# Optimization experiments

Measured on AMD Instinct MI355X. Metric: run time of the kernel, lower is better.

## Reference

```python
import jax, jax.numpy as jnp
import numpy as np

B, S, D, H = 2, 2048, 1024, 16
DK = D // H


def setup_inputs() -> dict:
    key = jax.random.key(0)
    ks = jax.random.split(key, 12)
    s = 0.02
    return {
        "q": jax.random.normal(ks[0], (B, S, D), jnp.float32),
        "k": jax.random.normal(ks[1], (B, S, D), jnp.float32),
        "v": jax.random.normal(ks[2], (B, S, D), jnp.float32),
        "mask": jax.random.randint(ks[3], (1, 1, S, S), 0, 2, jnp.int32),
        "Wq": jax.random.normal(ks[4], (D, D), jnp.float32) * s,
        "bq": jnp.zeros((D,), jnp.float32),
        "Wk": jax.random.normal(ks[5], (D, D), jnp.float32) * s,
        "bk": jnp.zeros((D,), jnp.float32),
        "Wv": jax.random.normal(ks[6], (D, D), jnp.float32) * s,
        "bv": jnp.zeros((D,), jnp.float32),
        "Wo": jax.random.normal(ks[7], (D, D), jnp.float32) * s,
        "bo": jnp.zeros((D,), jnp.float32),
    }


def reference(q, k, v, mask, Wq, bq, Wk, bk, Wv, bv, Wo, bo):
    # linear projections (torch Linear: x @ W.T + b)
    qp = q @ Wq.T + bq
    kp = k @ Wk.T + bk
    vp = v @ Wv.T + bv
    # [B, S, D] -> [B, H, S, DK]
    split = lambda x: x.reshape(B, S, H, DK).transpose(0, 2, 1, 3)
    qh, kh, vh = split(qp), split(kp), split(vp)
    scale = 1.0 / jnp.sqrt(jnp.float32(DK))
    attn = jnp.einsum('bhsd,bhtd->bhst', qh, kh) * scale  # [B,H,S,S]
    attn = jnp.where(mask == 0, jnp.float32(-1e9), attn)
    attn = jax.nn.softmax(attn, axis=-1)
    out = jnp.einsum('bhst,bhtd->bhsd', attn, vh)  # [B,H,S,DK]
    concat = out.transpose(0, 2, 1, 3).reshape(B, S, D)
    return concat @ Wo.T + bo
```

## Files before the change

### kernel.cpp

```cpp
#include <hip/hip_runtime.h>
#include <hip/hip_bf16.h>


using bf16x8 = __attribute__((ext_vector_type(8))) short;
using f32x4  = __attribute__((ext_vector_type(4))) float;

constexpr int Bc = 2, Sc = 2048, Dc = 1024, Hc = 16, DKc = 64;
constexpr int Mc = Bc * Sc;
#define QSCALE 0.18033688011112042f

__device__ __forceinline__ void lds_load16(const void* g, void* l) {
  __builtin_amdgcn_global_load_lds(
      (const __attribute__((address_space(1))) unsigned int*)g,
      (__attribute__((address_space(3))) unsigned int*)l, 16, 0, 0);
}

#if __has_builtin(__builtin_amdgcn_exp2f)
__device__ __forceinline__ float exp2_fast(float x) { return __builtin_amdgcn_exp2f(x); }
#else
__device__ __forceinline__ float exp2_fast(float x) {
  float r;
  asm("v_exp_f32 %0, %1\n\ts_nop 0" : "=v"(r) : "v"(x));
  return r;
}
#endif

__device__ __forceinline__ unsigned pack_trunc(float a, float b) {
  return __builtin_amdgcn_perm(__float_as_uint(b), __float_as_uint(a), 0x07060302u);
}

__device__ __forceinline__ unsigned pack2bf(float a, float b) {
  union { __hip_bfloat16 h; unsigned short s; } ua, ub;
  ua.h = __float2bfloat16(a);
  ub.h = __float2bfloat16(b);
  return (unsigned)ua.s | ((unsigned)ub.s << 16);
}

__global__ void cast3_kernel(const float* __restrict__ a, const float* __restrict__ b,
                             const float* __restrict__ c, __hip_bfloat16* __restrict__ oa,
                             __hip_bfloat16* __restrict__ ob, __hip_bfloat16* __restrict__ oc2,
                             int n) {
  int gid = blockIdx.x * blockDim.x + threadIdx.x;
  int per = n >> 2;
  int which = gid / per, i = (gid - which * per) * 4;
  const float* s = which == 0 ? a : (which == 1 ? b : c);
  __hip_bfloat16* d = which == 0 ? oa : (which == 1 ? ob : oc2);
  float4 x = *(const float4*)&s[i];
  d[i + 0] = __float2bfloat16(x.x);
  d[i + 1] = __float2bfloat16(x.y);
  d[i + 2] = __float2bfloat16(x.z);
  d[i + 3] = __float2bfloat16(x.w);
}

__global__ void cast4_kernel(const float* __restrict__ a, const float* __restrict__ b,
                             const float* __restrict__ c, const float* __restrict__ dd,
                             __hip_bfloat16* __restrict__ oa, __hip_bfloat16* __restrict__ ob,
                             __hip_bfloat16* __restrict__ oc2, __hip_bfloat16* __restrict__ od,
                             int n) {
  int gid = blockIdx.x * blockDim.x + threadIdx.x;
  int per = n >> 2;
  int which = gid / per, i = (gid - which * per) * 4;
  const float* s = which == 0 ? a : (which == 1 ? b : (which == 2 ? c : dd));
  __hip_bfloat16* d = which == 0 ? oa : (which == 1 ? ob : (which == 2 ? oc2 : od));
  float4 x = *(const float4*)&s[i];
  d[i + 0] = __float2bfloat16(x.x);
  d[i + 1] = __float2bfloat16(x.y);
  d[i + 2] = __float2bfloat16(x.z);
  d[i + 3] = __float2bfloat16(x.w);
}

__global__ void mask_pack_kernel(const int* __restrict__ mask,
                                 unsigned long long* __restrict__ bits) {
  int i = blockIdx.x * blockDim.x + threadIdx.x;
  unsigned long long bal = __ballot(mask[i] != 0);
  if ((threadIdx.x & 63) == 0) bits[i >> 6] = bal;
}

__global__ __launch_bounds__(256, 3) void proj_qkv(
    const __hip_bfloat16* __restrict__ qb, const __hip_bfloat16* __restrict__ kb,
    const __hip_bfloat16* __restrict__ vb, const __hip_bfloat16* __restrict__ Wcat,
    const float* __restrict__ bq, const float* __restrict__ bk,
    const float* __restrict__ bv, __hip_bfloat16* __restrict__ qhd,
    __hip_bfloat16* __restrict__ khd, __hip_bfloat16* __restrict__ vtd) {
  __shared__ __align__(16) __hip_bfloat16 As[128 * 64];
  __shared__ __align__(16) __hip_bfloat16 Bs[128 * 64];
  const int tid = threadIdx.x;
  const int m0 = blockIdx.x * 128, n0 = blockIdx.y * 128;
  const int which = n0 >> 10, nl0 = n0 & 1023;
  const __hip_bfloat16* X = which == 0 ? qb : (which == 1 ? kb : vb);
  const float* bias = which == 0 ? bq : (which == 1 ? bk : bv);
  const int w = tid >> 6, lane = tid & 63, ln = lane & 15, quad = lane >> 4;
  const int swz = ((lane & 7) ^ (lane >> 3)) * 8;
  const int rk0 = ln * 128 + ((quad ^ (ln & 7)) * 16);
  const int rk1 = ln * 128 + (((quad + 4) ^ (ln & 7)) * 16);
  const int aoff = (m0 + w * 32 + (lane >> 3)) * 1024 + swz;
  const int boff = (n0 + w * 32 + (lane >> 3)) * 1024 + swz;
  char* aF = (char*)As + (w >> 1) * 8192;
  char* bF = (char*)Bs + (w & 1) * 8192;
  char* aDst = (char*)As + w * 4096 + lane * 16;
  char* bDst = (char*)Bs + w * 4096 + lane * 16;
  f32x4 acc[4][4] = {};
  int ko = 0;
  for (int kb64 = 0; kb64 < 16; ++kb64, ko += 64) {
#pragma unroll
    for (int i = 0; i < 4; ++i) {
      lds_load16(&X[aoff + i * 8192 + ko], aDst + i * 1024);
      lds_load16(&Wcat[boff + i * 8192 + ko], bDst + i * 1024);
    }
    __syncthreads();
    bf16x8 af[4][2], bf[4][2];
#pragma unroll
    for (int i = 0; i < 4; ++i) {
      af[i][0] = *(bf16x8*)(aF + i * 2048 + rk0);
      af[i][1] = *(bf16x8*)(aF + i * 2048 + rk1);
      bf[i][0] = *(bf16x8*)(bF + i * 2048 + rk0);
      bf[i][1] = *(bf16x8*)(bF + i * 2048 + rk1);
    }
#pragma unroll
    for (int i = 0; i < 4; ++i)
#pragma unroll
      for (int j = 0; j < 4; ++j) {
        acc[i][j] = __builtin_amdgcn_mfma_f32_16x16x32_bf16(af[i][0], bf[j][0],
                                                            acc[i][j], 0, 0, 0);
        acc[i][j] = __builtin_amdgcn_mfma_f32_16x16x32_bf16(af[i][1], bf[j][1],
                                                            acc[i][j], 0, 0, 0);
      }
    __syncthreads();
  }
  const int wm = (w >> 1) * 64, wn = (w & 1) * 64;
#pragma unroll
  for (int i = 0; i < 4; ++i)
#pragma unroll
    for (int j = 0; j < 4; ++j) {
      int ngl = nl0 + wn + j * 16 + ln;
      int mbase = m0 + wm + i * 16 + quad * 4;
      float bb = bias[ngl];
      float vv[4];
#pragma unroll
      for (int r = 0; r < 4; ++r) vv[r] = acc[i][j][r] + bb;
      int h = ngl >> 6, dk = ngl & 63;
      int b = mbase >> 11, s = mbase & 2047;
      if (which == 0) {
#pragma unroll
        for (int r = 0; r < 4; ++r)
          qhd[(((size_t)(b * Hc + h) * Sc + s + r) * DKc) + dk] =
              __float2bfloat16(vv[r] * QSCALE);
      } else if (which == 1) {
#pragma unroll
        for (int r = 0; r < 4; ++r)
          khd[(((size_t)(b * Hc + h) * Sc + s + r) * DKc) + dk] =
              __float2bfloat16(vv[r]);
      } else {
        uint2 pk = {pack2bf(vv[0], vv[1]), pack2bf(vv[2], vv[3])};
        *(uint2*)&vtd[(((size_t)(b * Hc + h) * DKc + dk) * Sc) + s] = pk;
      }
    }
}

__global__ __launch_bounds__(256, 2) void gemm_out(
    const __hip_bfloat16* __restrict__ X, const __hip_bfloat16* __restrict__ W,
    const float* __restrict__ bias, float* __restrict__ Y) {
  __shared__ __align__(16) __hip_bfloat16 As[2][128 * 64];
  __shared__ __align__(16) __hip_bfloat16 Bs[2][64 * 64];
  const int tid = threadIdx.x;
  const int m0 = blockIdx.x * 128, n0 = blockIdx.y * 64;
  const int w = tid >> 6, lane = tid & 63, ln = lane & 15, quad = lane >> 4;
  const int wm = (w >> 1) * 64, wn = (w & 1) * 32;
  const int swz = ((lane & 7) ^ (lane >> 3)) * 8;
  const int rk0 = ln * 128 + ((quad ^ (ln & 7)) * 16);
  const int rk1 = ln * 128 + (((quad + 4) ^ (ln & 7)) * 16);
  const int aoff = (m0 + w * 32 + (lane >> 3)) * 1024 + swz;
  const int boff = (n0 + w * 16 + (lane >> 3)) * 1024 + swz;
  f32x4 acc[4][2] = {};

#define OSTAGE(KO, BI)                                                        \
  {                                                                           \
    _Pragma("unroll") for (int i = 0; i < 4; ++i)                             \
        lds_load16(&X[aoff + i * 8192 + (KO)],                                \
                   (char*)As[BI] + w * 4096 + lane * 16 + i * 1024);          \
    _Pragma("unroll") for (int i = 0; i < 2; ++i)                             \
        lds_load16(&W[boff + i * 8192 + (KO)],                                \
                   (char*)Bs[BI] + w * 2048 + lane * 16 + i * 1024);          \
  }

  OSTAGE(0, 0);
  for (int kb64 = 0; kb64 < 16; ++kb64) {
    const int bi = kb64 & 1;
    __syncthreads();
    if (kb64 + 1 < 16) OSTAGE((kb64 + 1) * 64, bi ^ 1);
    bf16x8 af[4][2], bf[2][2];
#pragma unroll
    for (int i = 0; i < 4; ++i) {
      af[i][0] = *(bf16x8*)((char*)As[bi] + wm * 128 + i * 2048 + rk0);
      af[i][1] = *(bf16x8*)((char*)As[bi] + wm * 128 + i * 2048 + rk1);
    }
#pragma unroll
    for (int j = 0; j < 2; ++j) {
      bf[j][0] = *(bf16x8*)((char*)Bs[bi] + wn * 128 + j * 2048 + rk0);
      bf[j][1] = *(bf16x8*)((char*)Bs[bi] + wn * 128 + j * 2048 + rk1);
    }
#pragma unroll
    for (int i = 0; i < 4; ++i)
#pragma unroll
      for (int j = 0; j < 2; ++j) {
        acc[i][j] = __builtin_amdgcn_mfma_f32_16x16x32_bf16(af[i][0], bf[j][0],
                                                            acc[i][j], 0, 0, 0);
        acc[i][j] = __builtin_amdgcn_mfma_f32_16x16x32_bf16(af[i][1], bf[j][1],
                                                            acc[i][j], 0, 0, 0);
      }
  }
#pragma unroll
  for (int i = 0; i < 4; ++i)
#pragma unroll
    for (int j = 0; j < 2; ++j) {
      int ng = n0 + wn + j * 16 + ln;
      int mbase = m0 + wm + i * 16 + quad * 4;
      float bb = bias[ng];
#pragma unroll
      for (int r = 0; r < 4; ++r)
        Y[(size_t)(mbase + r) * Dc + ng] = acc[i][j][r] + bb;
    }
}

__global__ __launch_bounds__(256, 2) void flash_attn(
    const __hip_bfloat16* __restrict__ qh, const __hip_bfloat16* __restrict__ kh,
    const __hip_bfloat16* __restrict__ vt, const uint4* __restrict__ mb4,
    __hip_bfloat16* __restrict__ oc) {
  __shared__ __align__(16) char L[51200];
  const int tid = threadIdx.x;
  const int bh = blockIdx.y, b = bh >> 4, h = bh & 15;
  const int q0 = blockIdx.x * 128;
  const int w = tid >> 6, lane = tid & 63, ln = lane & 15, quad = lane >> 4;
  const size_t base = (size_t)bh * Sc * DKc;
  const __hip_bfloat16* khb = kh + base;
  const __hip_bfloat16* vtb = vt + base;

  bf16x8 qf[2][2];
#pragma unroll
  for (int qt = 0; qt < 2; ++qt)
#pragma unroll
    for (int kc = 0; kc < 2; ++kc)
      qf[qt][kc] = *(const bf16x8*)&qh[base +
          (size_t)(q0 + w * 32 + qt * 16 + ln) * 64 + kc * 32 + quad * 8];

  const int swz = ((lane & 7) ^ (lane >> 3)) * 8;
  const int rk0 = ln * 128 + ((quad ^ (ln & 7)) * 16);
  const int rk1 = ln * 128 + (((quad + 4) ^ (ln & 7)) * 16);
  const int rPw = 32768 + w * 4608 + ln * 144 + quad * 8;
  const int rPb = 32768 + w * 4608 + ln * 144 + quad * 16;
  char* dmaL = L + w * 2048 + lane * 16;
  int koff = (w * 16 + (lane >> 3)) * 64 + swz;
  int voff0 = (w * 16 + (lane >> 3)) * Sc + swz;
  int voff1 = voff0 + 8 * Sc;
  int midx0 = (q0 + w * 32 + ln) * 16;
  int midx1 = midx0 + 256;
  const int sh0 = quad * 4, sh1 = quad * 4 + 16;

#define KV_DMA(BI)                                                            \
  {                                                                           \
    lds_load16(khb + koff, dmaL + (BI)*8192);                                 \
    lds_load16(khb + koff + 512, dmaL + (BI)*8192 + 1024);                    \
    lds_load16(vtb + voff0, dmaL + 16384 + (BI)*8192);                        \
    lds_load16(vtb + voff1, dmaL + 16384 + (BI)*8192 + 1024);                 \
  }

  float lsum[2] = {0.f, 0.f};
  f32x4 Oacc[4][2] = {};
  KV_DMA(0);

#define FTILE(BUF, LO0, HI0, LO1, HI1)                                        \
  {                                                                           \
    bf16x8 kf[4][2];                                                          \
    _Pragma("unroll") for (int tt = 0; tt < 4; ++tt) {                        \
      kf[tt][0] = *(bf16x8*)(L + (BUF)*8192 + tt * 2048 + rk0);               \
      kf[tt][1] = *(bf16x8*)(L + (BUF)*8192 + tt * 2048 + rk1);               \
    }                                                                         \
    _Pragma("unroll") for (int qt = 0; qt < 2; ++qt) {                        \
      f32x4 s[4];                                                             \
      _Pragma("unroll") for (int tt = 0; tt < 4; ++tt) {                      \
        f32x4 z = {0.f, 0.f, 0.f, 0.f};                                       \
        z = __builtin_amdgcn_mfma_f32_16x16x32_bf16(kf[tt][0], qf[qt][0], z,  \
                                                    0, 0, 0);                 \
        s[tt] = __builtin_amdgcn_mfma_f32_16x16x32_bf16(kf[tt][1], qf[qt][1], \
                                                        z, 0, 0, 0);          \
      }                                                                       \
      unsigned lo = qt ? (LO1) : (LO0), hi = qt ? (HI1) : (HI0);              \
      _Pragma("unroll") for (int tt = 0; tt < 4; ++tt) {                      \
        unsigned word = (tt & 2) ? hi : lo;                                   \
        unsigned pre = word >> ((tt & 1) ? sh1 : sh0);                        \
        float p[4];                                                           \
        _Pragma("unroll") for (int r = 0; r < 4; ++r) {                       \
          float e = exp2_fast(s[tt][r]);                                      \
          p[r] = (pre & (1u << r)) ? e : 0.f;                                 \
          lsum[qt] += p[r];                                                   \
        }                                                                     \
        uint2 pk = {pack_trunc(p[0], p[1]), pack_trunc(p[2], p[3])};          \
        *(uint2*)(L + rPw + qt * 2304 + tt * 32) = pk;                        \
      }                                                                       \
    }                                                                         \
    bf16x8 vf[4][2], pb[2][2];                                                \
    _Pragma("unroll") for (int dt = 0; dt < 4; ++dt) {                        \
      vf[dt][0] = *(bf16x8*)(L + 16384 + (BUF)*8192 + dt * 2048 + rk0);       \
      vf[dt][1] = *(bf16x8*)(L + 16384 + (BUF)*8192 + dt * 2048 + rk1);       \
    }                                                                         \
    _Pragma("unroll") for (int qt = 0; qt < 2; ++qt) {                        \
      pb[qt][0] = *(bf16x8*)(L + rPb + qt * 2304);                            \
      pb[qt][1] = *(bf16x8*)(L + rPb + qt * 2304 + 64);                       \
    }                                                                         \
    _Pragma("unroll") for (int dt = 0; dt < 4; ++dt)                          \
        _Pragma("unroll") for (int qt = 0; qt < 2; ++qt) {                    \
      Oacc[dt][qt] = __builtin_amdgcn_mfma_f32_16x16x32_bf16(                 \
          vf[dt][0], pb[qt][0], Oacc[dt][qt], 0, 0, 0);                       \
      Oacc[dt][qt] = __builtin_amdgcn_mfma_f32_16x16x32_bf16(                 \
          vf[dt][1], pb[qt][1], Oacc[dt][qt], 0, 0, 0);                       \
    }                                                                         \
  }

  for (int it2 = 0; it2 < 16; ++it2) {
    __syncthreads();
    uint4 mq0 = mb4[midx0], mq1 = mb4[midx1];
    ++midx0; ++midx1;
    koff += 4096; voff0 += 64; voff1 += 64;
    KV_DMA(1);
    FTILE(0, mq0.x, mq0.y, mq1.x, mq1.y);
    __syncthreads();
    if (it2 < 15) {
      koff += 4096; voff0 += 64; voff1 += 64;
      KV_DMA(0);
    }
    FTILE(1, mq0.z, mq0.w, mq1.z, mq1.w);
  }

  float linv[2];
#pragma unroll
  for (int qt = 0; qt < 2; ++qt) {
    float l = lsum[qt];
    l += __shfl_xor(l, 16);
    l += __shfl_xor(l, 32);
    linv[qt] = 1.f / fmaxf(l, 1e-30f);
  }
#pragma unroll
  for (int dt = 0; dt < 4; ++dt)
#pragma unroll
    for (int qt = 0; qt < 2; ++qt) {
      f32x4 o = Oacc[dt][qt];
      uint2 pk = {pack2bf(o[0] * linv[qt], o[1] * linv[qt]),
                  pack2bf(o[2] * linv[qt], o[3] * linv[qt])};
      *(uint2*)(L + rPw + qt * 2304 + dt * 32) = pk;
    }
  __builtin_amdgcn_s_waitcnt(0);
#pragma unroll
  for (int chunk = 0; chunk < 4; ++chunk) {
    int row = chunk * 8 + (lane >> 3);
    bf16x8 val = *(bf16x8*)(L + 32768 + w * 4608 + row * 144 + (lane & 7) * 16);
    int s = q0 + w * 32 + row;
    *(bf16x8*)&oc[(size_t)(b * Sc + s) * Dc + h * 64 + (lane & 7) * 8] = val;
  }
}

extern "C" void kernel_launch(void* const* d_in, const int* in_sizes, int n_in,
                              void* d_out, int out_size, void* d_ws, size_t ws_size,
                              hipStream_t stream) {
  const float* q  = (const float*)d_in[0];
  const float* k  = (const float*)d_in[1];
  const float* v  = (const float*)d_in[2];
  const int* mask = (const int*)d_in[3];
  const float* Wq = (const float*)d_in[4];
  const float* bq = (const float*)d_in[5];
  const float* Wk = (const float*)d_in[6];
  const float* bk = (const float*)d_in[7];
  const float* Wv = (const float*)d_in[8];
  const float* bv = (const float*)d_in[9];
  const float* Wo = (const float*)d_in[10];
  const float* bo = (const float*)d_in[11];

  char* ws = (char*)d_ws;
  const size_t MB = 1024 * 1024;
  __hip_bfloat16* qb  = (__hip_bfloat16*)(ws + 0 * MB);
  __hip_bfloat16* kb  = (__hip_bfloat16*)(ws + 8 * MB);
  unsigned long long* mbits = (unsigned long long*)(ws + 8 * MB);
  __hip_bfloat16* vb  = (__hip_bfloat16*)(ws + 16 * MB);
  __hip_bfloat16* Wqb = (__hip_bfloat16*)(ws + 24 * MB);
  __hip_bfloat16* Wkb = (__hip_bfloat16*)(ws + 26 * MB);
  __hip_bfloat16* Wvb = (__hip_bfloat16*)(ws + 28 * MB);
  __hip_bfloat16* Wob = (__hip_bfloat16*)(ws + 30 * MB);
  __hip_bfloat16* qhd = (__hip_bfloat16*)(ws + 32 * MB);
  __hip_bfloat16* khd = (__hip_bfloat16*)(ws + 40 * MB);
  __hip_bfloat16* vtd = (__hip_bfloat16*)(ws + 48 * MB);
  __hip_bfloat16* oc  = (__hip_bfloat16*)(ws + 56 * MB);

  const int nQKV = Mc * Dc, nW = Dc * Dc;
  cast3_kernel<<<3 * (nQKV / 4) / 256, 256, 0, stream>>>(q, k, v, qb, kb, vb, nQKV);
  cast4_kernel<<<4 * (nW / 4) / 256, 256, 0, stream>>>(Wq, Wk, Wv, Wo, Wqb, Wkb,
                                                       Wvb, Wob, nW);

  proj_qkv<<<dim3(Mc / 128, 3 * Dc / 128), 256, 0, stream>>>(
      qb, kb, vb, Wqb, bq, bk, bv, qhd, khd, vtd);

  mask_pack_kernel<<<(Sc * Sc) / 256, 256, 0, stream>>>(mask, mbits);

  flash_attn<<<dim3(Sc / 128, Bc * Hc), 256, 0, stream>>>(
      qhd, khd, vtd, (const uint4*)mbits, oc);

  gemm_out<<<dim3(Mc / 128, Dc / 64), 256, 0, stream>>>(oc, Wob, bo, (float*)d_out);
}
```

Before: 251.3 us.

## Split attention KV range across blocks, fuse prep kernels, remap grids

Fuses the three cast and mask-pack kernels into one prep launch. Splits the attention key range in two halves so twice as many blocks run, and writes fp32 partial outputs and row sums that a new reduce kernel combines and normalizes. Row sums are now computed with an MFMA against a ones vector instead of scalar adds. Remaps block indices in the projection, attention and output GEMMs into grouped 1D grids for cache locality, and raises flash_attn occupancy to 3 blocks per SM. This adds fp32 partial-result traffic and one extra launch in exchange for better occupancy and fewer small kernels.

```diff
diff --git a/kernel.cpp b/kernel.cpp
--- a/kernel.cpp
+++ b/kernel.cpp
@@ -36,44 +36,37 @@
   return (unsigned)ua.s | ((unsigned)ub.s << 16);
 }
 
-__global__ void cast3_kernel(const float* __restrict__ a, const float* __restrict__ b,
-                             const float* __restrict__ c, __hip_bfloat16* __restrict__ oa,
-                             __hip_bfloat16* __restrict__ ob, __hip_bfloat16* __restrict__ oc2,
-                             int n) {
-  int gid = blockIdx.x * blockDim.x + threadIdx.x;
-  int per = n >> 2;
-  int which = gid / per, i = (gid - which * per) * 4;
-  const float* s = which == 0 ? a : (which == 1 ? b : c);
-  __hip_bfloat16* d = which == 0 ? oa : (which == 1 ? ob : oc2);
-  float4 x = *(const float4*)&s[i];
-  d[i + 0] = __float2bfloat16(x.x);
-  d[i + 1] = __float2bfloat16(x.y);
-  d[i + 2] = __float2bfloat16(x.z);
-  d[i + 3] = __float2bfloat16(x.w);
-}
-
-__global__ void cast4_kernel(const float* __restrict__ a, const float* __restrict__ b,
-                             const float* __restrict__ c, const float* __restrict__ dd,
-                             __hip_bfloat16* __restrict__ oa, __hip_bfloat16* __restrict__ ob,
-                             __hip_bfloat16* __restrict__ oc2, __hip_bfloat16* __restrict__ od,
-                             int n) {
-  int gid = blockIdx.x * blockDim.x + threadIdx.x;
-  int per = n >> 2;
-  int which = gid / per, i = (gid - which * per) * 4;
-  const float* s = which == 0 ? a : (which == 1 ? b : (which == 2 ? c : dd));
-  __hip_bfloat16* d = which == 0 ? oa : (which == 1 ? ob : (which == 2 ? oc2 : od));
-  float4 x = *(const float4*)&s[i];
-  d[i + 0] = __float2bfloat16(x.x);
-  d[i + 1] = __float2bfloat16(x.y);
-  d[i + 2] = __float2bfloat16(x.z);
-  d[i + 3] = __float2bfloat16(x.w);
-}
-
-__global__ void mask_pack_kernel(const int* __restrict__ mask,
-                                 unsigned long long* __restrict__ bits) {
-  int i = blockIdx.x * blockDim.x + threadIdx.x;
-  unsigned long long bal = __ballot(mask[i] != 0);
-  if ((threadIdx.x & 63) == 0) bits[i >> 6] = bal;
+__global__ void prep(const float* __restrict__ q, const float* __restrict__ k,
+                     const float* __restrict__ v, const int* __restrict__ mask,
+                     const float* __restrict__ Wq, const float* __restrict__ Wk,
+                     const float* __restrict__ Wv, const float* __restrict__ Wo,
+                     char* __restrict__ ws) {
+  const size_t MB = 1024 * 1024;
+  int blk = blockIdx.x;
+  if (blk < 12288) {
+    int which = blk >> 12;
+    int i = (((blk & 4095) << 8) + threadIdx.x) * 4;
+    const float* s = which == 0 ? q : (which == 1 ? k : v);
+    __hip_bfloat16* d = (__hip_bfloat16*)(ws + (size_t)which * 8 * MB);
+    float4 x = *(const float4*)&s[i];
+    uint2 pk = {pack2bf(x.x, x.y), pack2bf(x.z, x.w)};
+    *(uint2*)&d[i] = pk;
+  } else if (blk < 16384) {
+    int bb = blk - 12288;
+    int which = bb >> 10;
+    int i = (((bb & 1023) << 8) + threadIdx.x) * 4;
+    const float* s = which == 0 ? Wq : (which == 1 ? Wk : (which == 2 ? Wv : Wo));
+    __hip_bfloat16* d = which < 3 ? (__hip_bfloat16*)(ws + (24 + 2 * which) * MB)
+                                  : (__hip_bfloat16*)(ws + 32 * MB);
+    float4 x = *(const float4*)&s[i];
+    uint2 pk = {pack2bf(x.x, x.y), pack2bf(x.z, x.w)};
+    *(uint2*)&d[i] = pk;
+  } else {
+    int i = ((blk - 16384) << 8) + threadIdx.x;
+    unsigned long long bal = __ballot(mask[i] != 0);
+    if ((threadIdx.x & 63) == 0)
+      ((unsigned long long*)(ws + 34 * MB))[i >> 6] = bal;
+  }
 }
 
 __global__ __launch_bounds__(256, 3) void proj_qkv(
@@ -85,7 +78,9 @@
   __shared__ __align__(16) __hip_bfloat16 As[128 * 64];
   __shared__ __align__(16) __hip_bfloat16 Bs[128 * 64];
   const int tid = threadIdx.x;
-  const int m0 = blockIdx.x * 128, n0 = blockIdx.y * 128;
+  const int f = blockIdx.x, g = f >> 3;
+  const int m0 = ((f & 7) * 4 + g / 24) * 128;
+  const int n0 = (g % 24) * 128;
   const int which = n0 >> 10, nl0 = n0 & 1023;
   const __hip_bfloat16* X = which == 0 ? qb : (which == 1 ? kb : vb);
   const float* bias = which == 0 ? bq : (which == 1 ? bk : bv);
@@ -163,7 +158,9 @@
   __shared__ __align__(16) __hip_bfloat16 As[2][128 * 64];
   __shared__ __align__(16) __hip_bfloat16 Bs[2][64 * 64];
   const int tid = threadIdx.x;
-  const int m0 = blockIdx.x * 128, n0 = blockIdx.y * 64;
+  const int f = blockIdx.x, g = f >> 3;
+  const int m0 = ((f & 7) * 4 + (g >> 4)) * 128;
+  const int n0 = (g & 15) * 64;
   const int w = tid >> 6, lane = tid & 63, ln = lane & 15, quad = lane >> 4;
   const int wm = (w >> 1) * 64, wn = (w & 1) * 32;
   const int swz = ((lane & 7) ^ (lane >> 3)) * 8;
@@ -222,17 +219,19 @@
     }
 }
 
-__global__ __launch_bounds__(256, 2) void flash_attn(
+__global__ __launch_bounds__(256, 3) void flash_attn(
     const __hip_bfloat16* __restrict__ qh, const __hip_bfloat16* __restrict__ kh,
     const __hip_bfloat16* __restrict__ vt, const uint4* __restrict__ mb4,
-    __hip_bfloat16* __restrict__ oc) {
+    float* __restrict__ opart, float* __restrict__ lpart) {
   __shared__ __align__(16) char L[51200];
   const int tid = threadIdx.x;
-  const int bh = blockIdx.y, b = bh >> 4, h = bh & 15;
-  const int q0 = blockIdx.x * 128;
+  const int f = blockIdx.x, g = f >> 3;
+  const int bhh = (f & 7) * 8 + (g >> 4);
+  const int q0 = (g & 15) * 128;
+  const int half = bhh >> 5, bh = bhh & 31;
   const int w = tid >> 6, lane = tid & 63, ln = lane & 15, quad = lane >> 4;
   const size_t base = (size_t)bh * Sc * DKc;
-  const __hip_bfloat16* khb = kh + base;
+  const __hip_bfloat16* khb = kh + base + half * 65536;
   const __hip_bfloat16* vtb = vt + base;
 
   bf16x8 qf[2][2];
@@ -242,6 +241,10 @@
     for (int kc = 0; kc < 2; ++kc)
       qf[qt][kc] = *(const bf16x8*)&qh[base +
           (size_t)(q0 + w * 32 + qt * 16 + ln) * 64 + kc * 32 + quad * 8];
+
+  bf16x8 onesA;
+#pragma unroll
+  for (int i = 0; i < 8; ++i) onesA[i] = (short)0x3F80;
 
   const int swz = ((lane & 7) ^ (lane >> 3)) * 8;
   const int rk0 = ln * 128 + ((quad ^ (ln & 7)) * 16);
@@ -250,9 +253,9 @@
   const int rPb = 32768 + w * 4608 + ln * 144 + quad * 16;
   char* dmaL = L + w * 2048 + lane * 16;
   int koff = (w * 16 + (lane >> 3)) * 64 + swz;
-  int voff0 = (w * 16 + (lane >> 3)) * Sc + swz;
+  int voff0 = (w * 16 + (lane >> 3)) * Sc + swz + half * 1024;
   int voff1 = voff0 + 8 * Sc;
-  int midx0 = (q0 + w * 32 + ln) * 16;
+  int midx0 = (q0 + w * 32 + ln) * 16 + half * 8;
   int midx1 = midx0 + 256;
   const int sh0 = quad * 4, sh1 = quad * 4 + 16;
 
@@ -264,8 +267,8 @@
     lds_load16(vtb + voff1, dmaL + 16384 + (BI)*8192 + 1024);                 \
   }
 
-  float lsum[2] = {0.f, 0.f};
   f32x4 Oacc[4][2] = {};
+  f32x4 lacc[2] = {};
   KV_DMA(0);
 
 #define FTILE(BUF, LO0, HI0, LO1, HI1)                                        \
@@ -292,7 +295,6 @@
         _Pragma("unroll") for (int r = 0; r < 4; ++r) {                       \
           float e = exp2_fast(s[tt][r]);                                      \
           p[r] = (pre & (1u << r)) ? e : 0.f;                                 \
-          lsum[qt] += p[r];                                                   \
         }                                                                     \
         uint2 pk = {pack_trunc(p[0], p[1]), pack_trunc(p[2], p[3])};          \
         *(uint2*)(L + rPw + qt * 2304 + tt * 32) = pk;                        \
@@ -306,6 +308,12 @@
     _Pragma("unroll") for (int qt = 0; qt < 2; ++qt) {                        \
       pb[qt][0] = *(bf16x8*)(L + rPb + qt * 2304);                            \
       pb[qt][1] = *(bf16x8*)(L + rPb + qt * 2304 + 64);                       \
+    }                                                                         \
+    _Pragma("unroll") for (int qt = 0; qt < 2; ++qt) {                        \
+      lacc[qt] = __builtin_amdgcn_mfma_f32_16x16x32_bf16(onesA, pb[qt][0],    \
+                                                         lacc[qt], 0, 0, 0);  \
+      lacc[qt] = __builtin_amdgcn_mfma_f32_16x16x32_bf16(onesA, pb[qt][1],    \
+                                                         lacc[qt], 0, 0, 0);  \
     }                                                                         \
     _Pragma("unroll") for (int dt = 0; dt < 4; ++dt)                          \
         _Pragma("unroll") for (int qt = 0; qt < 2; ++qt) {                    \
@@ -316,7 +324,7 @@
     }                                                                         \
   }
 
-  for (int it2 = 0; it2 < 16; ++it2) {
+  for (int it2 = 0; it2 < 8; ++it2) {
     __syncthreads();
     uint4 mq0 = mb4[midx0], mq1 = mb4[midx1];
     ++midx0; ++midx1;
@@ -324,38 +332,45 @@
     KV_DMA(1);
     FTILE(0, mq0.x, mq0.y, mq1.x, mq1.y);
     __syncthreads();
-    if (it2 < 15) {
+    if (it2 < 7) {
       koff += 4096; voff0 += 64; voff1 += 64;
       KV_DMA(0);
     }
     FTILE(1, mq0.z, mq0.w, mq1.z, mq1.w);
   }
 
-  float linv[2];
+  const size_t obase = (size_t)(half * 32 + bh) * 2048;
 #pragma unroll
   for (int qt = 0; qt < 2; ++qt) {
-    float l = lsum[qt];
-    l += __shfl_xor(l, 16);
-    l += __shfl_xor(l, 32);
-    linv[qt] = 1.f / fmaxf(l, 1e-30f);
-  }
-#pragma unroll
-  for (int dt = 0; dt < 4; ++dt)
-#pragma unroll
-    for (int qt = 0; qt < 2; ++qt) {
+    int qrow = q0 + w * 32 + qt * 16 + ln;
+#pragma unroll
+    for (int dt = 0; dt < 4; ++dt) {
       f32x4 o = Oacc[dt][qt];
-      uint2 pk = {pack2bf(o[0] * linv[qt], o[1] * linv[qt]),
-                  pack2bf(o[2] * linv[qt], o[3] * linv[qt])};
-      *(uint2*)(L + rPw + qt * 2304 + dt * 32) = pk;
-    }
-  __builtin_amdgcn_s_waitcnt(0);
-#pragma unroll
-  for (int chunk = 0; chunk < 4; ++chunk) {
-    int row = chunk * 8 + (lane >> 3);
-    bf16x8 val = *(bf16x8*)(L + 32768 + w * 4608 + row * 144 + (lane & 7) * 16);
-    int s = q0 + w * 32 + row;
-    *(bf16x8*)&oc[(size_t)(b * Sc + s) * Dc + h * 64 + (lane & 7) * 8] = val;
-  }
+      float4 st = {o[0], o[1], o[2], o[3]};
+      *(float4*)&opart[(obase + qrow) * 64 + dt * 16 + quad * 4] = st;
+    }
+    if (quad == 0) lpart[obase + qrow] = lacc[qt][0];
+  }
+}
+
+__global__ void reduce_o(const float* __restrict__ opart,
+                         const float* __restrict__ lpart,
+                         __hip_bfloat16* __restrict__ oc) {
+  int t = blockIdx.x * 256 + threadIdx.x;
+  int r = t >> 3, dk8 = (t & 7) * 8;
+  const size_t HS = (size_t)32 * 2048 * 64;
+  float4 a0 = *(const float4*)&opart[(size_t)r * 64 + dk8];
+  float4 a1 = *(const float4*)&opart[(size_t)r * 64 + dk8 + 4];
+  float4 b0 = *(const float4*)&opart[HS + (size_t)r * 64 + dk8];
+  float4 b1 = *(const float4*)&opart[HS + (size_t)r * 64 + dk8 + 4];
+  float li = 1.f / fmaxf(lpart[r] + lpart[65536 + r], 1e-30f);
+  int bh = r >> 11, qq = r & 2047, b = bh >> 4, h = bh & 15;
+  uint4 o;
+  o.x = pack2bf((a0.x + b0.x) * li, (a0.y + b0.y) * li);
+  o.y = pack2bf((a0.z + b0.z) * li, (a0.w + b0.w) * li);
+  o.z = pack2bf((a1.x + b1.x) * li, (a1.y + b1.y) * li);
+  o.w = pack2bf((a1.z + b1.z) * li, (a1.w + b1.w) * li);
+  *(uint4*)&oc[((size_t)(b * Sc + qq) * Dc) + h * 64 + dk8] = o;
 }
 
 extern "C" void kernel_launch(void* const* d_in, const int* in_sizes, int n_in,
@@ -376,31 +391,22 @@
 
   char* ws = (char*)d_ws;
   const size_t MB = 1024 * 1024;
-  __hip_bfloat16* qb  = (__hip_bfloat16*)(ws + 0 * MB);
-  __hip_bfloat16* kb  = (__hip_bfloat16*)(ws + 8 * MB);
-  unsigned long long* mbits = (unsigned long long*)(ws + 8 * MB);
-  __hip_bfloat16* vb  = (__hip_bfloat16*)(ws + 16 * MB);
-  __hip_bfloat16* Wqb = (__hip_bfloat16*)(ws + 24 * MB);
-  __hip_bfloat16* Wkb = (__hip_bfloat16*)(ws + 26 * MB);
-  __hip_bfloat16* Wvb = (__hip_bfloat16*)(ws + 28 * MB);
-  __hip_bfloat16* Wob = (__hip_bfloat16*)(ws + 30 * MB);
-  __hip_bfloat16* qhd = (__hip_bfloat16*)(ws + 32 * MB);
-  __hip_bfloat16* khd = (__hip_bfloat16*)(ws + 40 * MB);
-  __hip_bfloat16* vtd = (__hip_bfloat16*)(ws + 48 * MB);
-  __hip_bfloat16* oc  = (__hip_bfloat16*)(ws + 56 * MB);
-
-  const int nQKV = Mc * Dc, nW = Dc * Dc;
-  cast3_kernel<<<3 * (nQKV / 4) / 256, 256, 0, stream>>>(q, k, v, qb, kb, vb, nQKV);
-  cast4_kernel<<<4 * (nW / 4) / 256, 256, 0, stream>>>(Wq, Wk, Wv, Wo, Wqb, Wkb,
-                                                       Wvb, Wob, nW);
-
-  proj_qkv<<<dim3(Mc / 128, 3 * Dc / 128), 256, 0, stream>>>(
-      qb, kb, vb, Wqb, bq, bk, bv, qhd, khd, vtd);
-
-  mask_pack_kernel<<<(Sc * Sc) / 256, 256, 0, stream>>>(mask, mbits);
-
-  flash_attn<<<dim3(Sc / 128, Bc * Hc), 256, 0, stream>>>(
-      qhd, khd, vtd, (const uint4*)mbits, oc);
-
-  gemm_out<<<dim3(Mc / 128, Dc / 64), 256, 0, stream>>>(oc, Wob, bo, (float*)d_out);
-}
+  __hip_bfloat16* qb   = (__hip_bfloat16*)(ws + 0 * MB);
+  __hip_bfloat16* kb   = (__hip_bfloat16*)(ws + 8 * MB);
+  __hip_bfloat16* vb   = (__hip_bfloat16*)(ws + 16 * MB);
+  __hip_bfloat16* Wcat = (__hip_bfloat16*)(ws + 24 * MB);
+  float*          opart = (float*)(ws + 0 * MB);
+  __hip_bfloat16* Wob  = (__hip_bfloat16*)(ws + 32 * MB);
+  uint4*          mb4  = (uint4*)(ws + 34 * MB);
+  float*          lpart = (float*)(ws + 34 * MB + 512 * 1024);
+  __hip_bfloat16* qhd  = (__hip_bfloat16*)(ws + 35 * MB);
+  __hip_bfloat16* oc   = (__hip_bfloat16*)(ws + 35 * MB);
+  __hip_bfloat16* khd  = (__hip_bfloat16*)(ws + 43 * MB);
+  __hip_bfloat16* vtd  = (__hip_bfloat16*)(ws + 51 * MB);
+
+  prep<<<32768, 256, 0, stream>>>(q, k, v, mask, Wq, Wk, Wv, Wo, ws);
+  proj_qkv<<<768, 256, 0, stream>>>(qb, kb, vb, Wcat, bq, bk, bv, qhd, khd, vtd);
+  flash_attn<<<1024, 256, 0, stream>>>(qhd, khd, vtd, mb4, opart, lpart);
+  reduce_o<<<2048, 256, 0, stream>>>(opart, lpart, oc);
+  gemm_out<<<512, 256, 0, stream>>>(oc, Wob, bo, (float*)d_out);
+}
```

Measured after the change: 245.4 us. -2.4%, faster.
